# Kernel tuning notes

Hardware: AMD Instinct MI355X
Metric: run time of the kernel (lower is better)

The kernel has to match this reference:

```python
import jax, jax.numpy as jnp
import numpy as np

C = 1.0          # Poincare ball curvature
EPS = 1e-15
N, K, X, H = 16384, 16, 256, 256

def _artanh(x):
    return jnp.arctanh(jnp.clip(x, -1 + 1e-5, 1 - 1e-5))

def _norm(x):
    return jnp.sqrt(jnp.clip(jnp.sum(x * x, -1, keepdims=True), EPS))

def _proj(x):
    n = _norm(x)
    maxn = (1.0 - 1e-5) / np.sqrt(C)
    return jnp.where(n > maxn, x / n * maxn, x)

def mobius_add(x, y):
    x2 = jnp.sum(x * x, -1, keepdims=True)
    y2 = jnp.sum(y * y, -1, keepdims=True)
    xy = jnp.sum(x * y, -1, keepdims=True)
    num = (1 + 2 * C * xy + C * y2) * x + (1 - C * x2) * y
    den = 1 + 2 * C * xy + C * C * x2 * y2
    return _proj(num / jnp.clip(den, EPS))

def expmap0(u):
    sc = np.sqrt(C); un = _norm(u)
    return _proj(jnp.tanh(sc * un) * u / (sc * un))

def logmap0(x):
    sc = np.sqrt(C); xn = _norm(x)
    return _artanh(sc * xn) * x / (sc * xn)

def mobius_matvec(M, x):
    sc = np.sqrt(C); xn = _norm(x)
    mx = x @ M.T
    mxn = _norm(mx)
    return _proj(jnp.tanh(mxn / xn * _artanh(sc * xn)) * mx / (mxn * sc))

def mobius_pointwise_mul(w, x):
    # geoopt order: norm taken on x, product w*x
    sc = np.sqrt(C); xn = _norm(x)
    wx = w * x
    wxn = _norm(wx)
    return _proj(jnp.tanh(wxn / xn * _artanh(sc * xn)) * wx / (wxn * sc))

def mobius_scalar_mul(r, x):
    sc = np.sqrt(C); xn = _norm(x)
    return _proj(jnp.tanh(r * _artanh(sc * xn)) * x / (xn * sc))

def weighted_midpoint(x, axis):
    # geoopt weighted_midpoint with uniform weights, reducedim=[axis]
    lam = 2.0 / jnp.clip(1 - C * jnp.sum(x * x, -1, keepdims=True), EPS)
    num = jnp.sum(lam * x, axis=axis)
    den = jnp.sum(lam - 1.0, axis=axis)
    den = jnp.where(jnp.abs(den) < 1e-10, 1e-10, den)
    return mobius_scalar_mul(0.5, num / den)

def hyper_attn(h_, x_, g_t):
    # tangent-space scaled dot-product attention with Hawkes-decay bias
    q = logmap0(x_)                                   # [N,h]
    k = logmap0(h_)                                   # [N,K,h]
    logits = jnp.einsum('nkh,nh->nk', k, q) / np.sqrt(k.shape[-1]) + g_t
    return jax.nn.softmax(logits, axis=-1)            # [N,K]

def setup_inputs() -> dict:
    key = jax.random.key(0)
    ks = jax.random.split(key, 12)
    stdv = 1.0 / np.sqrt(H)
    u = lambda k, s: jax.random.uniform(k, s, jnp.float32, -stdv, stdv)
    return dict(
        x=0.5 * jax.random.normal(ks[0], (N, X), jnp.float32),
        h1=expmap0(0.05 * jax.random.normal(ks[1], (N, H), jnp.float32)),
        c1=expmap0(0.05 * jax.random.normal(ks[2], (N, H), jnp.float32)),
        del_t=10.0 * jax.random.uniform(ks[3], (N,), jnp.float32),
        edges=jax.random.randint(ks[4], (N, K), 0, N),
        W_iou=u(ks[5], (3 * H, X)), U_iou=u(ks[6], (3 * H, H)), b_iou=jnp.zeros((1, 3 * H)),
        U_f=u(ks[7], (H, H)),
        W_q=u(ks[8], (H, X)), b_q=jnp.zeros((1, H)),
        W_k=u(ks[9], (H, H)), b_k=jnp.zeros((1, H)),
        W_c=u(ks[10], (H, H)), b_c=jnp.zeros((1, H)),
        b_haw=jnp.array([1e-6], jnp.float32), a_haw=jnp.array([0.02], jnp.float32),
        haw_1=jnp.array([1.0], jnp.float32), haw_2=jnp.array([1.0], jnp.float32),
    )

def reference(x, h1, c1, del_t, edges, W_iou, U_iou, b_iou, U_f, W_q, b_q, W_k, b_k, W_c, b_c, b_haw, a_haw, haw_1, haw_2):
    Hm = h1[edges]                     # mailbox h1  [N,K,h]
    Cm = c1[edges]                     # mailbox c1  [N,K,h]
    dt = del_t[edges]                  # mailbox del_t [N,K]
    g_t = b_haw * jnp.exp(-a_haw * dt)                       # [N,K]
    x_ball = expmap0(x)
    # --- reduce_func ---
    x_q = mobius_add(mobius_matvec(W_q, x_ball), b_q)         # [N,h]
    h_k = mobius_add(mobius_matvec(W_k, Hm), b_k)             # [N,K,h]
    scores = hyper_attn(h_k, x_q, g_t)                        # [N,K]
    h_scaled = mobius_pointwise_mul(scores[..., None], Hm)
    decay = jnp.exp(-haw_2 * dt / 60.0)[..., None]
    h_max = mobius_pointwise_mul(jax.nn.relu(h_scaled), decay)
    h_hawkes = mobius_add(h_scaled, haw_1 * h_max)
    h_tild = weighted_midpoint(h_hawkes, axis=1)              # [N,h]
    c_sk = expmap0(jnp.tanh(logmap0(mobius_add(mobius_matvec(W_c, Cm), b_c))))
    c_sk_hat = mobius_pointwise_mul(c_sk, g_t[..., None])
    c_k_tilde = mobius_add(mobius_add(-c_sk, Cm), c_sk_hat)
    f = jax.nn.sigmoid(logmap0(mobius_matvec(U_f, Hm)))
    c_red = weighted_midpoint(mobius_pointwise_mul(f, c_k_tilde), axis=1)
    iou0 = mobius_matvec(W_iou, x_ball)                       # [N,3h]
    iou1 = mobius_add(iou0, mobius_matvec(U_iou, h_tild))
    # --- apply_node_func ---
    iou = mobius_add(iou1, b_iou)
    i, o, u2 = jnp.split(iou, 3, axis=1)
    i = jax.nn.sigmoid(logmap0(i))
    o = jax.nn.sigmoid(logmap0(o))
    u2 = jnp.tanh(logmap0(u2))
    c_new = mobius_add(mobius_pointwise_mul(i, u2), c_red)
    h_new = mobius_pointwise_mul(o, jnp.tanh(logmap0(c_new)))
    return h_new, c_new
```

## Files before the change

kernel.cpp:

```cpp
#include <hip/hip_runtime.h>
#include <math.h>

#define NN 16384
#define D  256
#define NB (NN*D)
#define EPSR 1e-15f
#define SQEPS 3.1622776601683794e-8f
#define MXN 0.99999f

typedef unsigned short u16;
typedef __bf16 bf16x8 __attribute__((ext_vector_type(8)));
typedef float f32x4 __attribute__((ext_vector_type(4)));
typedef unsigned short u16x8 __attribute__((ext_vector_type(8)));
typedef unsigned short u16x4 __attribute__((ext_vector_type(4)));

__device__ __forceinline__ float fexp(float x){ return __builtin_amdgcn_exp2f(x * 1.4426950408889634f); }
__device__ __forceinline__ float flog(float x){ return __builtin_amdgcn_logf(x) * 0.6931471805599453f; }
__device__ __forceinline__ float frcp(float x){ return __builtin_amdgcn_rcpf(x); }
__device__ __forceinline__ float fsqrt(float x){ return __builtin_amdgcn_sqrtf(x); }
__device__ __forceinline__ float ftanh(float x){
  float xc = fminf(fmaxf(x, -15.f), 15.f);
  float t = fexp(2.f * xc);
  return (t - 1.f) * frcp(t + 1.f);
}
__device__ __forceinline__ float at_c(float x){
  float xc = fminf(fmaxf(x, -1.f + 1e-5f), 1.f - 1e-5f);
  return 0.5f * flog((1.f + xc) * frcp(1.f - xc));
}
__device__ __forceinline__ float fsig(float x){ return frcp(1.f + fexp(-x)); }

__device__ __forceinline__ float b2f(u16 u){
  unsigned int x = ((unsigned int)u) << 16;
  return __builtin_bit_cast(float, x);
}
__device__ __forceinline__ u16 f2b(float f){
  unsigned int u = __builtin_bit_cast(unsigned int, f);
  return (u16)((u + 0x7fffu + ((u >> 16) & 1u)) >> 16);
}
__device__ __forceinline__ float wred(float v){
#pragma unroll
  for (int m = 32; m; m >>= 1) v += __shfl_xor(v, m);
  return v;
}
__device__ __forceinline__ float sig_proj(float npre, float* nrm){
  float n = fmaxf(npre, SQEPS);
  float s = (n > MXN) ? (MXN * frcp(n)) : 1.f;
  *nrm = fminf(n, MXN);
  return s;
}
__device__ __forceinline__ void ld4(const u16* p, float v[4]){
  u16x4 t = *(const u16x4*)p;
#pragma unroll
  for (int r = 0; r < 4; r++) v[r] = b2f(t[r]);
}
__device__ __forceinline__ void ld4f(const float* p, float v[4]){
  f32x4 t = *(const f32x4*)p;
#pragma unroll
  for (int r = 0; r < 4; r++) v[r] = t[r];
}

__global__ void __launch_bounds__(256) k_wcvt(
    const float* __restrict__ Wq, const float* __restrict__ Wiou,
    const float* __restrict__ Wk, const float* __restrict__ Uf,
    const float* __restrict__ Wc, const float* __restrict__ Uiou,
    u16* __restrict__ dst)
{
  size_t base = ((size_t)blockIdx.x * 256 + threadIdx.x) * 4;
  const float* src; size_t off;
  if      (base <  65536){ src = Wq;   off = base; }
  else if (base < 262144){ src = Wiou; off = base - 65536; }
  else if (base < 327680){ src = Wk;   off = base - 262144; }
  else if (base < 393216){ src = Uf;   off = base - 327680; }
  else if (base < 458752){ src = Wc;   off = base - 393216; }
  else                   { src = Uiou; off = base - 458752; }
  f32x4 v = *(const f32x4*)(src + off);
  u16x4 o;
#pragma unroll
  for (int r = 0; r < 4; r++) o[r] = f2b(v[r]);
  *(u16x4*)(dst + base) = o;
}

__global__ void __launch_bounds__(256) k_prep(const float* __restrict__ x,
    const float* __restrict__ h1, const float* __restrict__ c1,
    u16* __restrict__ xbb, u16* __restrict__ cb, u16* __restrict__ pack,
    float* __restrict__ scal)
{
  int w = threadIdx.x >> 6, lane = threadIdx.x & 63;
  int n = blockIdx.x * 4 + w;
  int base = n * D + lane * 4;
  float xv[4], hv[4], cv[4];
  ld4f(x + base, xv); ld4f(h1 + base, hv); ld4f(c1 + base, cv);
  float un2 = 0, hn2 = 0, prn2 = 0, cn2 = 0;
#pragma unroll
  for (int r = 0; r < 4; r++){
    un2 += xv[r]*xv[r]; hn2 += hv[r]*hv[r];
    float rr = fmaxf(hv[r], 0.f); prn2 += rr*rr;
    cn2 += cv[r]*cv[r];
  }
  un2 = wred(un2); hn2 = wred(hn2); prn2 = wred(prn2); cn2 = wred(cn2);
  float un = fsqrt(fmaxf(un2, EPSR));
  float t  = ftanh(un);
  float sc = t * frcp(un);
  float nx = fsqrt(fmaxf(sc*sc*un2, EPSR));
  float s  = (nx > MXN) ? (MXN * frcp(nx)) : 1.f;
  u16x4 ox, oh, oc;
#pragma unroll
  for (int r = 0; r < 4; r++){ ox[r] = f2b(s*sc*xv[r]); oh[r] = f2b(hv[r]); oc[r] = f2b(cv[r]); }
  *(u16x4*)(xbb + base) = ox;
  *(u16x4*)(cb + base) = oc;
  *(u16x4*)(pack + (size_t)n*768 + lane*4) = oh;
  if (lane == 0){
    float* sp = scal + (size_t)n * 16;
    sp[0] = fminf(nx, MXN);
    sp[1] = hn2; sp[2] = prn2; sp[3] = cn2;
    float hn = fsqrt(fmaxf(hn2, EPSR));
    sp[9] = at_c(hn); sp[10] = hn;
  }
}

#define TM 128
#define TN 128
#define TK 32
#define LDP 40
__global__ void __launch_bounds__(256) gemm_bt(const u16* __restrict__ A, int lda,
    const u16* __restrict__ B, u16* __restrict__ C, int K, int Nout)
{
  __shared__ u16 As[TM*LDP];
  __shared__ u16 Bs[TN*LDP];
  int t = threadIdx.x;
  int m0 = blockIdx.x * TM, n0 = blockIdx.y * TN;
  int w = t >> 6, lane = t & 63;
  int wr = w >> 1, wc = w & 1;
  int q = lane >> 4, l16 = lane & 15;
  f32x4 acc[4][4];
#pragma unroll
  for (int i = 0; i < 4; i++)
#pragma unroll
    for (int j = 0; j < 4; j++) acc[i][j] = (f32x4){0.f,0.f,0.f,0.f};
  for (int k0 = 0; k0 < K; k0 += TK){
    __syncthreads();
#pragma unroll
    for (int c = t; c < 512; c += 256){
      int row = c >> 2, ko = (c & 3) * 8;
      *(u16x8*)(As + row*LDP + ko) = *(const u16x8*)(A + (size_t)(m0+row)*lda + k0 + ko);
      *(u16x8*)(Bs + row*LDP + ko) = *(const u16x8*)(B + (size_t)(n0+row)*K + k0 + ko);
    }
    __syncthreads();
    bf16x8 af[4], bfr[4];
#pragma unroll
    for (int rb = 0; rb < 4; rb++)
      af[rb] = *(const bf16x8*)(As + (wr*64 + rb*16 + l16)*LDP + q*8);
#pragma unroll
    for (int cb2 = 0; cb2 < 4; cb2++)
      bfr[cb2] = *(const bf16x8*)(Bs + (wc*64 + cb2*16 + l16)*LDP + q*8);
#pragma unroll
    for (int rb = 0; rb < 4; rb++)
#pragma unroll
      for (int cb2 = 0; cb2 < 4; cb2++)
        acc[rb][cb2] = __builtin_amdgcn_mfma_f32_16x16x32_bf16(af[rb], bfr[cb2], acc[rb][cb2], 0, 0, 0);
  }
#pragma unroll
  for (int rb = 0; rb < 4; rb++)
#pragma unroll
    for (int cb2 = 0; cb2 < 4; cb2++)
#pragma unroll
      for (int r = 0; r < 4; r++){
        int m  = m0 + wr*64 + rb*16 + q*4 + r;
        int nn = n0 + wc*64 + cb2*16 + l16;
        C[(size_t)m*Nout + nn] = f2b(acc[rb][cb2][r]);
      }
}

__device__ __forceinline__ float mm_madd(const float mv[4], const float bv[4], float xn, float z[4]){
  float mn2 = 0.f;
#pragma unroll
  for (int r = 0; r < 4; r++) mn2 += mv[r]*mv[r];
  mn2 = wred(mn2);
  float mnc = fsqrt(fmaxf(mn2, EPSR));
  float imnc = frcp(mnc);
  float t = ftanh(mnc * frcp(xn) * at_c(xn));
  float npre = t * fsqrt(mn2) * imnc;
  float nf; float sg = sig_proj(npre, &nf);
  float cx = sg * t * imnc;
  float x2 = (sg*npre)*(sg*npre);
  float y2 = 0.f, xy = 0.f;
#pragma unroll
  for (int r = 0; r < 4; r++){ y2 += bv[r]*bv[r]; xy += cx*mv[r]*bv[r]; }
  y2 = wred(y2); xy = wred(xy);
  float A = 1.f + 2.f*xy + y2, Bc = 1.f - x2;
  float idn = frcp(fmaxf(1.f + 2.f*xy + x2*y2, EPSR));
  float zn2 = (A*A*x2 + 2.f*A*Bc*xy + Bc*Bc*y2) * idn * idn;
  float zn = fsqrt(fmaxf(zn2, EPSR));
  float sz = (zn > MXN) ? (MXN * frcp(zn)) : 1.f;
  float ca = sz * A * idn * cx, cb = sz * Bc * idn;
#pragma unroll
  for (int r = 0; r < 4; r++) z[r] = ca*mv[r] + cb*bv[r];
  return fminf(zn, MXN);
}

__global__ void __launch_bounds__(256) k_post(
    const u16* __restrict__ mqiou, const u16* __restrict__ mkf,
    const u16* __restrict__ mc,
    const float* __restrict__ c1,
    const float* __restrict__ bq, const float* __restrict__ bk, const float* __restrict__ bc,
    u16* __restrict__ qv, u16* __restrict__ kv,
    u16* __restrict__ pack,
    float* __restrict__ scal)
{
  int w = threadIdx.x >> 6, lane = threadIdx.x & 63;
  int n = blockIdx.x * 4 + w;
  int base = n * D + lane * 4, lb = lane * 4;
  float* sp = scal + (size_t)n * 16;
  float xbn = sp[0], hn2 = sp[1], cn2 = sp[3];
  float hnc = fsqrt(fmaxf(hn2, EPSR));
  float cnc = fsqrt(fmaxf(cn2, EPSR));
  float mv[4], bv[4], z[4];
  u16x4 o;
  ld4(mqiou + (size_t)n*1024 + lb, mv); ld4f(bq + lb, bv);
  float znf = mm_madd(mv, bv, xbn, z);
  float cl = at_c(znf) * frcp(znf);
#pragma unroll
  for (int r = 0; r < 4; r++) o[r] = f2b(cl * z[r]);
  *(u16x4*)(qv + base) = o;
  ld4(mkf + (size_t)n*512 + lb, mv); ld4f(bk + lb, bv);
  znf = mm_madd(mv, bv, hnc, z);
  cl = at_c(znf) * frcp(znf);
#pragma unroll
  for (int r = 0; r < 4; r++) o[r] = f2b(cl * z[r]);
  *(u16x4*)(kv + base) = o;
  float fv[4];
  {
    ld4(mkf + (size_t)n*512 + 256 + lb, mv);
    float mn2 = 0.f;
#pragma unroll
    for (int r = 0; r < 4; r++) mn2 += mv[r]*mv[r];
    mn2 = wred(mn2);
    float mnc = fsqrt(fmaxf(mn2, EPSR));
    float imnc = frcp(mnc);
    float t = ftanh(mnc * frcp(hnc) * at_c(hnc));
    float npre = t * fsqrt(mn2) * imnc;
    float nf; float sg = sig_proj(npre, &nf);
    float cx = sg * t * imnc;
    float lcf = at_c(nf) * frcp(nf);
#pragma unroll
    for (int r = 0; r < 4; r++) fv[r] = fsig(lcf * cx * mv[r]);
  }
  float csk[4];
  {
    ld4(mc + base, mv); ld4f(bc + lb, bv);
    float zn = mm_madd(mv, bv, cnc, z);
    float lc = at_c(zn) * frcp(zn);
    float th[4]; float thn2 = 0.f;
#pragma unroll
    for (int r = 0; r < 4; r++){ th[r] = ftanh(lc * z[r]); thn2 += th[r]*th[r]; }
    thn2 = wred(thn2);
    float thn = fsqrt(fmaxf(thn2, EPSR));
    float te = ftanh(thn);
    float se = te * frcp(thn);
    float npe = fsqrt(fmaxf(se*se*thn2, EPSR));
    float sge = (npe > MXN) ? (MXN * frcp(npe)) : 1.f;
#pragma unroll
    for (int r = 0; r < 4; r++) csk[r] = sge * se * th[r];
  }
  float c1v[4]; ld4f(c1 + base, c1v);
  float csn2 = 0, pcc = 0, pfss = 0, pfsm = 0, pfmm = 0;
#pragma unroll
  for (int r = 0; r < 4; r++){
    float f2 = fv[r]*fv[r];
    csn2 += csk[r]*csk[r];
    pcc  += csk[r]*c1v[r];
    pfss += f2*csk[r]*csk[r];
    pfsm += f2*csk[r]*c1v[r];
    pfmm += f2*c1v[r]*c1v[r];
  }
  csn2 = wred(csn2); pcc = wred(pcc); pfss = wred(pfss); pfsm = wred(pfsm); pfmm = wred(pfmm);
  u16x4 oa, ob;
#pragma unroll
  for (int r = 0; r < 4; r++){ oa[r] = f2b(fv[r]*csk[r]); ob[r] = f2b(fv[r]*c1v[r]); }
  *(u16x4*)(pack + (size_t)n*768 + 256 + lb) = oa;
  *(u16x4*)(pack + (size_t)n*768 + 512 + lb) = ob;
  if (lane == 0){
    sp[4] = csn2; sp[5] = pcc; sp[6] = pfss; sp[7] = pfsm; sp[8] = pfmm;
  }
}

__global__ void __launch_bounds__(256) k_lgc(
    const int* __restrict__ edges, const float* __restrict__ del_t,
    const u16* __restrict__ qv, const u16* __restrict__ kvec,
    const float* __restrict__ scal,
    const float* __restrict__ pbh, const float* __restrict__ pah,
    const float* __restrict__ ph1, const float* __restrict__ ph2,
    float* __restrict__ coef)
{
  __shared__ int   s_j[4][16];
  __shared__ float s_dt[4][16];
  __shared__ float s_lg[4][16];
  int w = threadIdx.x >> 6, lane = threadIdx.x & 63;
  int n = blockIdx.x * 4 + w;
  float bh = pbh[0], ah = pah[0], hw1 = ph1[0], hw2 = ph2[0];
  float qf[4]; ld4(qv + n*D + lane*4, qf);
#pragma unroll
  for (int k = 0; k < 16; k++){
    int j = edges[n*16 + k];
    float dt = del_t[j];
    u16x4 kt = *(const u16x4*)(kvec + (size_t)j*D + lane*4);
    float d = 0.f;
#pragma unroll
    for (int r = 0; r < 4; r++) d += qf[r] * b2f(kt[r]);
    d = wred(d);
    if (lane == 0){ s_j[w][k] = j; s_dt[w][k] = dt; s_lg[w][k] = d * 0.0625f + bh * fexp(-ah * dt); }
  }
  __syncthreads();
  if (lane >= 16) return;
  int e = n*16 + lane;
  int j = s_j[w][lane];
  float dt = s_dt[w][lane];
  const float* ln = s_lg[w];
  float mxl = -1e30f;
#pragma unroll
  for (int k = 0; k < 16; k++) mxl = fmaxf(mxl, ln[k]);
  float sume = 0.f;
#pragma unroll
  for (int k = 0; k < 16; k++) sume += fexp(ln[k] - mxl);
  float sk = fexp(ln[lane] - mxl) * frcp(sume);
  const float* sp2 = scal + (size_t)j * 16;
  float hn2 = sp2[1], prn2 = sp2[2], cn2 = sp2[3], csn2 = sp2[4], pcc = sp2[5],
        pfss = sp2[6], pfsm = sp2[7], pfmm = sp2[8], athn = sp2[9], hn = sp2[10];
  float g = bh * fexp(-ah * dt);
  float decay = fexp(-hw2 * dt * (1.f/60.f));
  float wxn1 = fsqrt(fmaxf(sk*sk*hn2, EPSR));
  float iwxn1 = frcp(wxn1);
  float t1 = ftanh(wxn1 * frcp(hn) * athn);
  float npre1 = t1 * sk * fsqrt(hn2) * iwxn1;
  float nn1 = fmaxf(npre1, SQEPS); float sg1 = (nn1 > MXN) ? MXN*frcp(nn1) : 1.f;
  float a_h = sg1 * t1 * sk * iwxn1;
  float rn2 = a_h*a_h*prn2;
  float xnd  = fsqrt(fmaxf(decay*decay, EPSR));
  float wxn2 = fsqrt(fmaxf(decay*decay*rn2, EPSR));
  float iwxn2 = frcp(wxn2);
  float t2 = ftanh(wxn2 * frcp(xnd) * at_c(xnd));
  float npre2 = t2 * decay * fsqrt(rn2) * iwxn2;
  float nn2 = fmaxf(npre2, SQEPS); float sg2 = (nn2 > MXN) ? MXN*frcp(nn2) : 1.f;
  float b_h = sg2 * t2 * decay * a_h * iwxn2;
  float bh1 = hw1 * b_h;
  float x2 = a_h*a_h*hn2;
  float y2 = bh1*bh1*prn2;
  float xy = a_h*bh1*prn2;
  float A = 1.f + 2.f*xy + y2, B = 1.f - x2;
  float idn = frcp(fmaxf(1.f + 2.f*xy + x2*y2, EPSR));
  float nh2 = (A*A*x2 + 2.f*A*B*xy + B*B*y2) * idn * idn;
  float nh = fsqrt(fmaxf(nh2, EPSR)); float sg3 = (nh > MXN) ? MXN*frcp(nh) : 1.f;
  float p  = sg3 * A * a_h * idn;
  float rr = sg3 * B * bh1 * idn;
  float hhn2 = sg3*sg3*nh2;
  float lam = 2.f * frcp(fmaxf(1.f - hhn2, EPSR));
  float xng  = fsqrt(fmaxf(g*g, EPSR));
  float wxn3 = fsqrt(fmaxf(g*g*csn2, EPSR));
  float iwxn3 = frcp(wxn3);
  float t3 = ftanh(wxn3 * frcp(xng) * at_c(xng));
  float npre3 = t3 * g * fsqrt(csn2) * iwxn3;
  float nn3 = fmaxf(npre3, SQEPS); float sgc = (nn3 > MXN) ? MXN*frcp(nn3) : 1.f;
  float gam = sgc * t3 * g * iwxn3;
  float A1 = 1.f - 2.f*pcc + cn2, B1 = 1.f - csn2;
  float iden1 = frcp(fmaxf(1.f - 2.f*pcc + csn2*cn2, EPSR));
  float al = -A1*iden1, be = B1*iden1;
  float n1sq = al*al*csn2 + 2.f*al*be*pcc + be*be*cn2;
  float n1 = fsqrt(fmaxf(n1sq, EPSR)); float s1 = (n1 > MXN) ? MXN*frcp(n1) : 1.f;
  al *= s1; be *= s1;
  float z1n2 = s1*s1*n1sq;
  float y2c = gam*gam*csn2;
  float xyc = gam*(al*csn2 + be*pcc);
  float A2 = 1.f + 2.f*xyc + y2c, B2 = 1.f - z1n2;
  float iden2 = frcp(fmaxf(1.f + 2.f*xyc + z1n2*y2c, EPSR));
  float u1 = (A2*al + B2*gam)*iden2, u2 = A2*be*iden2;
  float n2sq = u1*u1*csn2 + 2.f*u1*u2*pcc + u2*u2*cn2;
  float n2 = fsqrt(fmaxf(n2sq, EPSR)); float s2 = (n2 > MXN) ? MXN*frcp(n2) : 1.f;
  u1 *= s2; u2 *= s2;
  float xnc = fminf(n2, MXN);
  float wx2 = u1*u1*pfss + 2.f*u1*u2*pfsm + u2*u2*pfmm;
  float wxn4 = fsqrt(fmaxf(wx2, EPSR));
  float iwxn4 = frcp(wxn4);
  float t4 = ftanh(wxn4 * frcp(xnc) * at_c(xnc));
  float npre4 = t4 * fsqrt(wx2) * iwxn4;
  float nn4 = fmaxf(npre4, SQEPS); float s4 = (nn4 > MXN) ? MXN*frcp(nn4) : 1.f;
  float v1 = s4*t4*u1*iwxn4, v2 = s4*t4*u2*iwxn4;
  float rsn2 = (s4*npre4)*(s4*npre4);
  float lam2 = 2.f * frcp(fmaxf(1.f - rsn2, EPSR));
  float* cf = coef + (size_t)e * 6;
  cf[0] = lam; cf[1] = lam*p; cf[2] = lam*rr;
  cf[3] = lam2; cf[4] = lam2*v1; cf[5] = lam2*v2;
}

__global__ void __launch_bounds__(256) k_acc(
    const int* __restrict__ edges, const u16* __restrict__ pack,
    const float* __restrict__ coef,
    u16* __restrict__ ht, u16* __restrict__ cred, float* __restrict__ htn_arr)
{
  __shared__ f32x4 s_nh[2][64];
  __shared__ f32x4 s_nc[2][64];
  __shared__ float s_d[2][2];
  int w = threadIdx.x >> 6, lane = threadIdx.x & 63;
  int nb = w >> 1, half = w & 1;
  int n = blockIdx.x * 2 + nb;
  float numh[4] = {0,0,0,0}, numc[4] = {0,0,0,0};
  float denh = 0.f, denc = 0.f;
#pragma unroll
  for (int kk = 0; kk < 8; kk++){
    int k = half*8 + kk;
    int e = n*16 + k;
    int j = edges[e];
    const float* cf = coef + (size_t)e * 6;
    float lam = cf[0], lamp = cf[1], lamr = cf[2];
    float lam2 = cf[3], lv1 = cf[4], lv2 = cf[5];
    denh += lam - 1.f; denc += lam2 - 1.f;
    const u16* pr = pack + (size_t)j*768 + lane*4;
    u16x4 hx4 = *(const u16x4*)(pr);
    u16x4 fs4 = *(const u16x4*)(pr + 256);
    u16x4 fm4 = *(const u16x4*)(pr + 512);
#pragma unroll
    for (int r = 0; r < 4; r++){
      float hxr = b2f(hx4[r]);
      numh[r] += lamp*hxr + lamr*fmaxf(hxr, 0.f);
      numc[r] += lv1*b2f(fs4[r]) + lv2*b2f(fm4[r]);
    }
  }
  if (half == 1){
    f32x4 a, b;
#pragma unroll
    for (int r = 0; r < 4; r++){ a[r] = numh[r]; b[r] = numc[r]; }
    s_nh[nb][lane] = a; s_nc[nb][lane] = b;
    if (lane == 0){ s_d[nb][0] = denh; s_d[nb][1] = denc; }
  }
  __syncthreads();
  if (half == 1) return;
  {
    f32x4 a = s_nh[nb][lane], b = s_nc[nb][lane];
#pragma unroll
    for (int r = 0; r < 4; r++){ numh[r] += a[r]; numc[r] += b[r]; }
    denh += s_d[nb][0]; denc += s_d[nb][1];
  }
  if (fabsf(denh) < 1e-10f) denh = 1e-10f;
  if (fabsf(denc) < 1e-10f) denc = 1e-10f;
  float idh = frcp(denh), idc = frcp(denc);
  float vh[4], vc[4]; float vn2h = 0.f, vn2c = 0.f;
#pragma unroll
  for (int r = 0; r < 4; r++){
    vh[r] = numh[r]*idh; vn2h += vh[r]*vh[r];
    vc[r] = numc[r]*idc; vn2c += vc[r]*vc[r];
  }
  vn2h = wred(vn2h); vn2c = wred(vn2c);
  float vnh = fsqrt(fmaxf(vn2h, EPSR));
  float tth = ftanh(0.5f * at_c(vnh));
  float nph = tth * fsqrt(vn2h) * frcp(vnh);
  float nfh; float sh = sig_proj(nph, &nfh);
  float chh = sh * tth * frcp(vnh);
  u16x4 ho;
#pragma unroll
  for (int r = 0; r < 4; r++) ho[r] = f2b(chh * vh[r]);
  *(u16x4*)(ht + (size_t)n*D + lane*4) = ho;
  if (lane == 0) htn_arr[n] = nfh;
  float vnc = fsqrt(fmaxf(vn2c, EPSR));
  float ttc = ftanh(0.5f * at_c(vnc));
  float npc = ttc * fsqrt(vn2c) * frcp(vnc);
  float nfc; float scz = sig_proj(npc, &nfc);
  float chc = scz * ttc * frcp(vnc);
  u16x4 co;
#pragma unroll
  for (int r = 0; r < 4; r++) co[r] = f2b(chc * vc[r]);
  *(u16x4*)(cred + (size_t)n*D + lane*4) = co;
}

__global__ void __launch_bounds__(256) k_final(
    const u16* __restrict__ mqiou, const u16* __restrict__ mu,
    const u16* __restrict__ cred, const float* __restrict__ biou,
    const float* __restrict__ scal, const float* __restrict__ htn_arr,
    float* __restrict__ out)
{
  int w = threadIdx.x >> 6, lane = threadIdx.x & 63;
  int n = blockIdx.x * 4 + w;
  float mi[3][4], muv[3][4], bi[3][4];
#pragma unroll
  for (int p = 0; p < 3; p++){
    ld4(mqiou + (size_t)n*1024 + 256 + p*256 + lane*4, mi[p]);
    ld4(mu   + (size_t)n*768 + p*256 + lane*4, muv[p]);
    ld4f(biou + p*256 + lane*4, bi[p]);
  }
  float cr[4]; ld4(cred + (size_t)n*D + lane*4, cr);
  float xbn = scal[(size_t)n*16 + 0];
  float htn = htn_arr[n];
  float mn2 = 0.f, un2 = 0.f, dmu = 0.f;
#pragma unroll
  for (int p = 0; p < 3; p++)
#pragma unroll
    for (int r = 0; r < 4; r++){
      mn2 += mi[p][r]*mi[p][r]; un2 += muv[p][r]*muv[p][r]; dmu += mi[p][r]*muv[p][r];
    }
  mn2 = wred(mn2); un2 = wred(un2); dmu = wred(dmu);
  float mnc = fsqrt(fmaxf(mn2, EPSR));
  float ta = ftanh(mnc * frcp(xbn) * at_c(xbn));
  float npa = ta * fsqrt(mn2) * frcp(mnc);
  float na_; float sa = sig_proj(npa, &na_);
  float ca = sa * ta * frcp(mnc); float x2 = (sa*npa)*(sa*npa);
  float unc = fsqrt(fmaxf(un2, EPSR));
  float tb = ftanh(unc * frcp(htn) * at_c(htn));
  float npb = tb * fsqrt(un2) * frcp(unc);
  float nb_; float sb = sig_proj(npb, &nb_);
  float cb = sb * tb * frcp(unc); float y2 = (sb*npb)*(sb*npb);
  float xy = ca * cb * dmu;
  float A = 1.f + 2.f*xy + y2, B = 1.f - x2;
  float idn = frcp(fmaxf(1.f + 2.f*xy + x2*y2, EPSR));
  float c_mi = A*ca*idn, c_mu = B*cb*idn;
  float n1sq = (A*A*x2 + 2.f*A*B*xy + B*B*y2) * idn * idn;
  float n1 = fsqrt(fmaxf(n1sq, EPSR)); float s1 = (n1 > MXN) ? MXN*frcp(n1) : 1.f;
  c_mi *= s1; c_mu *= s1;
  float iou1n2 = s1*s1*n1sq;
  float io1[3][4]; float bb2 = 0.f, xyb = 0.f;
#pragma unroll
  for (int p = 0; p < 3; p++)
#pragma unroll
    for (int r = 0; r < 4; r++){
      io1[p][r] = c_mi*mi[p][r] + c_mu*muv[p][r];
      bb2 += bi[p][r]*bi[p][r]; xyb += io1[p][r]*bi[p][r];
    }
  bb2 = wred(bb2); xyb = wred(xyb);
  float A2 = 1.f + 2.f*xyb + bb2, B2 = 1.f - iou1n2;
  float iden2 = frcp(fmaxf(1.f + 2.f*xyb + iou1n2*bb2, EPSR));
  float n2sq = (A2*A2*iou1n2 + 2.f*A2*B2*xyb + B2*B2*bb2) * iden2 * iden2;
  float n2c = fsqrt(fmaxf(n2sq, EPSR)); float s2 = (n2c > MXN) ? MXN*frcp(n2c) : 1.f;
  float cA2 = s2*A2*iden2, cB2 = s2*B2*iden2;
  float iou[3][4];
#pragma unroll
  for (int p = 0; p < 3; p++)
#pragma unroll
    for (int r = 0; r < 4; r++) iou[p][r] = cA2*io1[p][r] + cB2*bi[p][r];
  float ni2 = 0.f, no2 = 0.f, nu2 = 0.f;
#pragma unroll
  for (int r = 0; r < 4; r++){ ni2 += iou[0][r]*iou[0][r]; no2 += iou[1][r]*iou[1][r]; nu2 += iou[2][r]*iou[2][r]; }
  ni2 = wred(ni2); no2 = wred(no2); nu2 = wred(nu2);
  float niN = fsqrt(fmaxf(ni2, EPSR)), noN = fsqrt(fmaxf(no2, EPSR)), nuN = fsqrt(fmaxf(nu2, EPSR));
  float ci = at_c(niN)*frcp(niN), co = at_c(noN)*frcp(noN), cu = at_c(nuN)*frcp(nuN);
  float iv[4], ov[4], uv[4];
#pragma unroll
  for (int r = 0; r < 4; r++){
    iv[r] = fsig(ci*iou[0][r]);
    ov[r] = fsig(co*iou[1][r]);
    uv[r] = ftanh(cu*iou[2][r]);
  }
  float xn2 = 0.f, wn2 = 0.f; float wx[4];
#pragma unroll
  for (int r = 0; r < 4; r++){ xn2 += uv[r]*uv[r]; wx[r] = iv[r]*uv[r]; wn2 += wx[r]*wx[r]; }
  xn2 = wred(xn2); wn2 = wred(wn2);
  float xnc = fsqrt(fmaxf(xn2, EPSR)), wnc = fsqrt(fmaxf(wn2, EPSR));
  float t4 = ftanh(wnc * frcp(xnc) * at_c(xnc));
  float np4 = t4 * fsqrt(wn2) * frcp(wnc);
  float n4_; float s4 = sig_proj(np4, &n4_);
  float cpm = s4*t4*frcp(wnc); float pmn2 = (s4*np4)*(s4*np4);
  float y2c = 0.f, xyc = 0.f;
#pragma unroll
  for (int r = 0; r < 4; r++){ y2c += cr[r]*cr[r]; xyc += cpm*wx[r]*cr[r]; }
  y2c = wred(y2c); xyc = wred(xyc);
  float A3 = 1.f + 2.f*xyc + y2c, B3 = 1.f - pmn2;
  float iden3 = frcp(fmaxf(1.f + 2.f*xyc + pmn2*y2c, EPSR));
  float n3sq = (A3*A3*pmn2 + 2.f*A3*B3*xyc + B3*B3*y2c) * iden3 * iden3;
  float n3 = fsqrt(fmaxf(n3sq, EPSR)); float s3 = (n3 > MXN) ? MXN*frcp(n3) : 1.f;
  float cA3 = s3*A3*cpm*iden3, cB3 = s3*B3*iden3;
  float cnw[4]; f32x4 oc;
#pragma unroll
  for (int r = 0; r < 4; r++){ cnw[r] = cA3*wx[r] + cB3*cr[r]; oc[r] = cnw[r]; }
  *(f32x4*)(out + NB + (size_t)n*D + lane*4) = oc;
  float ncn = fminf(n3, MXN);
  float clg = at_c(ncn)*frcp(ncn);
  float th[4]; float xn5 = 0.f, wn5 = 0.f; float wx5[4];
#pragma unroll
  for (int r = 0; r < 4; r++){
    th[r] = ftanh(clg*cnw[r]);
    xn5 += th[r]*th[r]; wx5[r] = ov[r]*th[r]; wn5 += wx5[r]*wx5[r];
  }
  xn5 = wred(xn5); wn5 = wred(wn5);
  float xn5c = fsqrt(fmaxf(xn5, EPSR)), wn5c = fsqrt(fmaxf(wn5, EPSR));
  float t5 = ftanh(wn5c * frcp(xn5c) * at_c(xn5c));
  float np5 = t5 * fsqrt(wn5) * frcp(wn5c);
  float n5_; float s5 = sig_proj(np5, &n5_);
  float ch = s5*t5*frcp(wn5c);
  f32x4 oh;
#pragma unroll
  for (int r = 0; r < 4; r++) oh[r] = ch * wx5[r];
  *(f32x4*)(out + (size_t)n*D + lane*4) = oh;
}

extern "C" void kernel_launch(void* const* d_in, const int* in_sizes, int n_in,
                              void* d_out, int out_size, void* d_ws, size_t ws_size,
                              hipStream_t stream)
{
  (void)in_sizes; (void)n_in; (void)out_size; (void)ws_size;
  const float* x     = (const float*)d_in[0];
  const float* h1    = (const float*)d_in[1];
  const float* c1    = (const float*)d_in[2];
  const float* del_t = (const float*)d_in[3];
  const int*   edges = (const int*)d_in[4];
  const float* W_iou = (const float*)d_in[5];
  const float* U_iou = (const float*)d_in[6];
  const float* b_iou = (const float*)d_in[7];
  const float* U_f   = (const float*)d_in[8];
  const float* W_q   = (const float*)d_in[9];
  const float* b_q   = (const float*)d_in[10];
  const float* W_k   = (const float*)d_in[11];
  const float* b_k   = (const float*)d_in[12];
  const float* W_c   = (const float*)d_in[13];
  const float* b_c   = (const float*)d_in[14];
  const float* b_haw = (const float*)d_in[15];
  const float* a_haw = (const float*)d_in[16];
  const float* haw1  = (const float*)d_in[17];
  const float* haw2  = (const float*)d_in[18];

  u16* wb    = (u16*)d_ws;
  u16* xbb   = wb + 655360;
  u16* cb    = xbb + NB;
  u16* pack  = cb + NB;
  u16* mqiou = pack + (size_t)NN*768;
  u16* mkf   = mqiou + 4*(size_t)NB;
  u16* mc    = mkf + 2*(size_t)NB;
  u16* qv    = mc + NB;
  u16* kvec  = qv + NB;
  float* scal    = (float*)(kvec + NB);
  float* coefbuf = scal + (size_t)NN*16;
  float* htn_arr = coefbuf + (size_t)NN*96;
  u16* ht   = xbb;
  u16* cred = qv;
  u16* mu   = mkf;

  k_wcvt<<<640, 256, 0, stream>>>(W_q, W_iou, W_k, U_f, W_c, U_iou, wb);
  k_prep<<<NN/4, 256, 0, stream>>>(x, h1, c1, xbb, cb, pack, scal);
  gemm_bt<<<dim3(NN/128, 8), 256, 0, stream>>>(xbb, 256, wb,          mqiou, 256, 1024);
  gemm_bt<<<dim3(NN/128, 4), 256, 0, stream>>>(pack, 768, wb+262144,  mkf,   256, 512);
  gemm_bt<<<dim3(NN/128, 2), 256, 0, stream>>>(cb,  256, wb+393216,   mc,    256, 256);
  k_post<<<NN/4, 256, 0, stream>>>(mqiou, mkf, mc, c1, b_q, b_k, b_c, qv, kvec, pack, scal);
  k_lgc<<<NN/4, 256, 0, stream>>>(edges, del_t, qv, kvec, scal, b_haw, a_haw, haw1, haw2, coefbuf);
  k_acc<<<NN/2, 256, 0, stream>>>(edges, pack, coefbuf, ht, cred, htn_arr);
  gemm_bt<<<dim3(NN/128, 6), 256, 0, stream>>>(ht, 256, wb+458752, mu, 256, 768);
  k_final<<<NN/4, 256, 0, stream>>>(mqiou, mu, cred, b_iou, scal, htn_arr, (float*)d_out);
}
```

Before: 334.6 us.

## Use direct global-to-LDS loads with XOR swizzle and merge three GEMM launches

The GEMM tile loads now go straight from global memory into LDS through global_load_lds instead of staging through registers. The padded shared layout is replaced by an XOR-swizzled layout, which keeps fragment reads free of bank conflicts. The three independent projection GEMMs are merged into one launch with a 14-wide grid, which cuts launch overhead and fills the GPU better. The swizzle must match between the loader lanes and the readers, and K is now hardcoded to 256.

```diff
diff --git a/kernel.cpp b/kernel.cpp
--- a/kernel.cpp
+++ b/kernel.cpp
@@ -57,6 +57,11 @@
   f32x4 t = *(const f32x4*)p;
 #pragma unroll
   for (int r = 0; r < 4; r++) v[r] = t[r];
+}
+__device__ __forceinline__ void glds16(const u16* g, u16* l){
+  typedef __attribute__((address_space(1))) const unsigned int gu32;
+  typedef __attribute__((address_space(3))) unsigned int lu32;
+  __builtin_amdgcn_global_load_lds((gu32*)g, (lu32*)l, 16, 0, 0);
 }
 
 __global__ void __launch_bounds__(256) k_wcvt(
@@ -121,38 +126,49 @@
 #define TM 128
 #define TN 128
 #define TK 32
-#define LDP 40
-__global__ void __launch_bounds__(256) gemm_bt(const u16* __restrict__ A, int lda,
-    const u16* __restrict__ B, u16* __restrict__ C, int K, int Nout)
-{
-  __shared__ u16 As[TM*LDP];
-  __shared__ u16 Bs[TN*LDP];
+__device__ __forceinline__ void gemm_core(const u16* __restrict__ A, int lda,
+    const u16* __restrict__ B, u16* __restrict__ C, int Nout,
+    int m0, int n0, u16* As, u16* Bs)
+{
   int t = threadIdx.x;
-  int m0 = blockIdx.x * TM, n0 = blockIdx.y * TN;
   int w = t >> 6, lane = t & 63;
   int wr = w >> 1, wc = w & 1;
   int q = lane >> 4, l16 = lane & 15;
+  int lrow = lane >> 2, lc = lane & 3;
+  int r0 = w*32 + lrow, r1 = r0 + 16;
+  int cg0 = lc ^ (r0 & 3) ^ ((r0 >> 2) & 3);
+  int cg1 = lc ^ (r1 & 3) ^ ((r1 >> 2) & 3);
+  const u16* a0 = A + (size_t)(m0 + r0)*lda + cg0*8;
+  const u16* a1 = A + (size_t)(m0 + r1)*lda + cg1*8;
+  const u16* b0 = B + (size_t)(n0 + r0)*256 + cg0*8;
+  const u16* b1 = B + (size_t)(n0 + r1)*256 + cg1*8;
+  u16* lA0 = As + (w*32)*32;      u16* lA1 = As + (w*32 + 16)*32;
+  u16* lB0 = Bs + (w*32)*32;      u16* lB1 = Bs + (w*32 + 16)*32;
   f32x4 acc[4][4];
 #pragma unroll
   for (int i = 0; i < 4; i++)
 #pragma unroll
     for (int j = 0; j < 4; j++) acc[i][j] = (f32x4){0.f,0.f,0.f,0.f};
-  for (int k0 = 0; k0 < K; k0 += TK){
+  for (int k0 = 0; k0 < 256; k0 += TK){
     __syncthreads();
-#pragma unroll
-    for (int c = t; c < 512; c += 256){
-      int row = c >> 2, ko = (c & 3) * 8;
-      *(u16x8*)(As + row*LDP + ko) = *(const u16x8*)(A + (size_t)(m0+row)*lda + k0 + ko);
-      *(u16x8*)(Bs + row*LDP + ko) = *(const u16x8*)(B + (size_t)(n0+row)*K + k0 + ko);
-    }
+    glds16(a0 + k0, lA0);
+    glds16(a1 + k0, lA1);
+    glds16(b0 + k0, lB0);
+    glds16(b1 + k0, lB1);
     __syncthreads();
     bf16x8 af[4], bfr[4];
 #pragma unroll
-    for (int rb = 0; rb < 4; rb++)
-      af[rb] = *(const bf16x8*)(As + (wr*64 + rb*16 + l16)*LDP + q*8);
-#pragma unroll
-    for (int cb2 = 0; cb2 < 4; cb2++)
-      bfr[cb2] = *(const bf16x8*)(Bs + (wc*64 + cb2*16 + l16)*LDP + q*8);
+    for (int rb = 0; rb < 4; rb++){
+      int ra = wr*64 + rb*16 + l16;
+      int ca = q ^ (ra & 3) ^ ((ra >> 2) & 3);
+      af[rb] = *(const bf16x8*)(As + ra*32 + ca*8);
+    }
+#pragma unroll
+    for (int cb2 = 0; cb2 < 4; cb2++){
+      int rb2 = wc*64 + cb2*16 + l16;
+      int cbk = q ^ (rb2 & 3) ^ ((rb2 >> 2) & 3);
+      bfr[cb2] = *(const bf16x8*)(Bs + rb2*32 + cbk*8);
+    }
 #pragma unroll
     for (int rb = 0; rb < 4; rb++)
 #pragma unroll
@@ -169,6 +185,29 @@
         int nn = n0 + wc*64 + cb2*16 + l16;
         C[(size_t)m*Nout + nn] = f2b(acc[rb][cb2][r]);
       }
+}
+
+__global__ void __launch_bounds__(256) k_mm3(
+    const u16* __restrict__ xbb, const u16* __restrict__ pack,
+    const u16* __restrict__ cbp, const u16* __restrict__ wb,
+    u16* __restrict__ mqiou, u16* __restrict__ mkf, u16* __restrict__ mc)
+{
+  __shared__ u16 As[TM*32];
+  __shared__ u16 Bs[TN*32];
+  int by = blockIdx.y;
+  const u16* A; int lda; const u16* B; u16* C; int Nout; int n0;
+  if (by < 8)      { A = xbb;  lda = 256; B = wb;          C = mqiou; Nout = 1024; n0 = by*128; }
+  else if (by < 12){ A = pack; lda = 768; B = wb + 262144; C = mkf;   Nout = 512;  n0 = (by-8)*128; }
+  else             { A = cbp;  lda = 256; B = wb + 393216; C = mc;    Nout = 256;  n0 = (by-12)*128; }
+  gemm_core(A, lda, B, C, Nout, blockIdx.x*TM, n0, As, Bs);
+}
+
+__global__ void __launch_bounds__(256) gemm_bt(const u16* __restrict__ A, int lda,
+    const u16* __restrict__ B, u16* __restrict__ C, int Nout)
+{
+  __shared__ u16 As[TM*32];
+  __shared__ u16 Bs[TN*32];
+  gemm_core(A, lda, B, C, Nout, blockIdx.x*TM, blockIdx.y*TN, As, Bs);
 }
 
 __device__ __forceinline__ float mm_madd(const float mv[4], const float bv[4], float xn, float z[4]){
@@ -631,12 +670,10 @@
 
   k_wcvt<<<640, 256, 0, stream>>>(W_q, W_iou, W_k, U_f, W_c, U_iou, wb);
   k_prep<<<NN/4, 256, 0, stream>>>(x, h1, c1, xbb, cb, pack, scal);
-  gemm_bt<<<dim3(NN/128, 8), 256, 0, stream>>>(xbb, 256, wb,          mqiou, 256, 1024);
-  gemm_bt<<<dim3(NN/128, 4), 256, 0, stream>>>(pack, 768, wb+262144,  mkf,   256, 512);
-  gemm_bt<<<dim3(NN/128, 2), 256, 0, stream>>>(cb,  256, wb+393216,   mc,    256, 256);
+  k_mm3<<<dim3(NN/128, 14), 256, 0, stream>>>(xbb, pack, cb, wb, mqiou, mkf, mc);
   k_post<<<NN/4, 256, 0, stream>>>(mqiou, mkf, mc, c1, b_q, b_k, b_c, qv, kvec, pack, scal);
   k_lgc<<<NN/4, 256, 0, stream>>>(edges, del_t, qv, kvec, scal, b_haw, a_haw, haw1, haw2, coefbuf);
   k_acc<<<NN/2, 256, 0, stream>>>(edges, pack, coefbuf, ht, cred, htn_arr);
-  gemm_bt<<<dim3(NN/128, 6), 256, 0, stream>>>(ht, 256, wb+458752, mu, 256, 768);
+  gemm_bt<<<dim3(NN/128, 6), 256, 0, stream>>>(ht, 256, wb + 458752, mu, 768);
   k_final<<<NN/4, 256, 0, stream>>>(mqiou, mu, cred, b_iou, scal, htn_arr, (float*)d_out);
 }
```

Result: faster. 315.0 us (-5.9%).
